# Kernel tuning notes

Measured on AMD Instinct MI355X. Metric: run time of the kernel, lower is better.

Reference implementation:

```python
import jax, jax.numpy as jnp
import numpy as np

ALPHA = 0.2  # LeakyReLU negative slope
NEG_INF = -9e15


def setup_inputs() -> dict:
    key = jax.random.key(0)
    k_h, k_adj, k_W, k_a = jax.random.split(key, 4)
    B, N, Din, Dout = 8, 1024, 256, 256
    h = jax.random.normal(k_h, (B, N, Din), dtype=jnp.float32)
    adj = jax.random.randint(k_adj, (B, N, N), 0, 2, dtype=jnp.int32)
    # nn.Linear weight [out, in], xavier-uniform-ish init for a
    W = jax.random.normal(k_W, (Dout, Din), dtype=jnp.float32) * (1.0 / np.sqrt(Din))
    lim = np.float32(1.414 * np.sqrt(6.0 / (2 * Dout + 1)))
    a = jax.random.uniform(k_a, (2 * Dout, 1), dtype=jnp.float32, minval=-lim, maxval=lim)
    return {"h": h, "adj": adj, "W": W, "a": a}


def reference(h, adj, W, a):
    # Wh: [B, N, F]
    Wh = jnp.einsum('bnd,fd->bnf', h, W)
    F_ = Wh.shape[-1]
    # Decompose concat-then-matmul: e_ij = leakyrelu(Wh_i @ a1 + Wh_j @ a2)
    a1 = a[:F_, 0]   # [F]
    a2 = a[F_:, 0]   # [F]
    src = Wh @ a1    # [B, N]  score contribution of row node i
    dst = Wh @ a2    # [B, N]  score contribution of col node j
    e = src[:, :, None] + dst[:, None, :]          # [B, N, N]
    e = jnp.where(e > 0, e, ALPHA * e)             # LeakyReLU
    e = jnp.where(adj > 0, e, NEG_INF)             # mask non-edges
    attention = jax.nn.softmax(e, axis=-1)         # [B, N, N]
    # dropout p=0.0 -> identity in eval/train
    h_prime = jnp.einsum('bij,bjf->bif', attention, Wh)
    return h_prime
```

## Files before the change

kernel.cpp:

```cpp
#include <hip/hip_runtime.h>
#include <hip/hip_bf16.h>
#include <cstdint>

#define ALPHA 0.2f
#define NEG_INF -9000000000000000.0f

typedef __bf16 bf16_t;
typedef __bf16 bf16x8 __attribute__((ext_vector_type(8)));
typedef float f32x16 __attribute__((ext_vector_type(16)));

__global__ __launch_bounds__(256) void k_gemm1(
    const float* __restrict__ h, const float* __restrict__ W, bf16_t* __restrict__ WhT)
{
  __shared__ bf16_t WS[64 * 72];
  __shared__ bf16_t HS[64 * 72];
  const int bx = blockIdx.x;
  const int b  = bx & 7;
  const int jt = (bx >> 3) & 15;
  const int ft = bx >> 7;
  const int j0 = jt * 64, f0 = ft * 64;
  const int t = threadIdx.x;
  const int w = t >> 6, lane = t & 63;
  const int mrow = lane & 31, half = lane >> 5;
  const int fsub = (w & 1) * 32, jsub = (w >> 1) * 32;

  const int lr = t >> 2;
  const int lc = (t & 3) * 16;
  const float* wp = W + ((size_t)(f0 + lr)) * 256 + lc;
  const float* hp = h + ((size_t)(b * 1024 + j0 + lr)) * 256 + lc;

  f32x16 acc;
#pragma unroll
  for (int r = 0; r < 16; r++) acc[r] = 0.f;

  for (int s = 0; s < 4; s++) {
    if (s) __syncthreads();
    {
      float4 w0 = *(const float4*)(wp + s * 64);
      float4 w1 = *(const float4*)(wp + s * 64 + 4);
      float4 w2 = *(const float4*)(wp + s * 64 + 8);
      float4 w3 = *(const float4*)(wp + s * 64 + 12);
      bf16x8 va, vb;
      va[0] = (bf16_t)w0.x; va[1] = (bf16_t)w0.y; va[2] = (bf16_t)w0.z; va[3] = (bf16_t)w0.w;
      va[4] = (bf16_t)w1.x; va[5] = (bf16_t)w1.y; va[6] = (bf16_t)w1.z; va[7] = (bf16_t)w1.w;
      vb[0] = (bf16_t)w2.x; vb[1] = (bf16_t)w2.y; vb[2] = (bf16_t)w2.z; vb[3] = (bf16_t)w2.w;
      vb[4] = (bf16_t)w3.x; vb[5] = (bf16_t)w3.y; vb[6] = (bf16_t)w3.z; vb[7] = (bf16_t)w3.w;
      *(bf16x8*)&WS[lr * 72 + lc] = va;
      *(bf16x8*)&WS[lr * 72 + lc + 8] = vb;
      float4 h0 = *(const float4*)(hp + s * 64);
      float4 h1 = *(const float4*)(hp + s * 64 + 4);
      float4 h2 = *(const float4*)(hp + s * 64 + 8);
      float4 h3 = *(const float4*)(hp + s * 64 + 12);
      bf16x8 vc, vd;
      vc[0] = (bf16_t)h0.x; vc[1] = (bf16_t)h0.y; vc[2] = (bf16_t)h0.z; vc[3] = (bf16_t)h0.w;
      vc[4] = (bf16_t)h1.x; vc[5] = (bf16_t)h1.y; vc[6] = (bf16_t)h1.z; vc[7] = (bf16_t)h1.w;
      vd[0] = (bf16_t)h2.x; vd[1] = (bf16_t)h2.y; vd[2] = (bf16_t)h2.z; vd[3] = (bf16_t)h2.w;
      vd[4] = (bf16_t)h3.x; vd[5] = (bf16_t)h3.y; vd[6] = (bf16_t)h3.z; vd[7] = (bf16_t)h3.w;
      *(bf16x8*)&HS[lr * 72 + lc] = vc;
      *(bf16x8*)&HS[lr * 72 + lc + 8] = vd;
    }
    __syncthreads();
#pragma unroll
    for (int ks = 0; ks < 4; ks++) {
      bf16x8 af = *(const bf16x8*)&WS[(fsub + mrow) * 72 + ks * 16 + half * 8];
      bf16x8 bf = *(const bf16x8*)&HS[(jsub + mrow) * 72 + ks * 16 + half * 8];
      acc = __builtin_amdgcn_mfma_f32_32x32x16_bf16(af, bf, acc, 0, 0, 0);
    }
  }

  const int jcol = j0 + jsub + mrow;
#pragma unroll
  for (int r = 0; r < 16; r++) {
    int frow = fsub + (r & 3) + 8 * (r >> 2) + 4 * half;
    WhT[(((size_t)(b * 256 + f0 + frow)) << 10) + jcol] = (bf16_t)acc[r];
  }
}

__global__ __launch_bounds__(256) void k_src(
    const float* __restrict__ h, const float* __restrict__ W, const float* __restrict__ a,
    float* __restrict__ src, float* __restrict__ dst)
{
  __shared__ float uS[512];
  const int t = threadIdx.x;
  {
    float s1a = 0.f, s1b = 0.f, s2a = 0.f, s2b = 0.f;
#pragma unroll 4
    for (int f = 0; f < 256; f += 2) {
      float w0 = W[f * 256 + t];
      float w1 = W[(f + 1) * 256 + t];
      s1a = fmaf(w0, a[f], s1a);       s1b = fmaf(w1, a[f + 1], s1b);
      s2a = fmaf(w0, a[256 + f], s2a); s2b = fmaf(w1, a[256 + f + 1], s2b);
    }
    uS[t] = s1a + s1b; uS[256 + t] = s2a + s2b;
  }
  __syncthreads();
  const int n = t >> 4, c = t & 15;
  const int m = blockIdx.x * 16 + n;
  const float* hp = h + (size_t)m * 256 + c * 16;
  float s1 = 0.f, s2 = 0.f;
#pragma unroll
  for (int i = 0; i < 4; i++) {
    float4 v = *(const float4*)(hp + i * 4);
    const float* u1p = &uS[c * 16 + i * 4];
    const float* u2p = &uS[256 + c * 16 + i * 4];
    s1 = fmaf(v.x, u1p[0], s1); s1 = fmaf(v.y, u1p[1], s1);
    s1 = fmaf(v.z, u1p[2], s1); s1 = fmaf(v.w, u1p[3], s1);
    s2 = fmaf(v.x, u2p[0], s2); s2 = fmaf(v.y, u2p[1], s2);
    s2 = fmaf(v.z, u2p[2], s2); s2 = fmaf(v.w, u2p[3], s2);
  }
#pragma unroll
  for (int off = 8; off; off >>= 1) {
    s1 += __shfl_down(s1, off, 16);
    s2 += __shfl_down(s2, off, 16);
  }
  if (c == 0) { src[m] = s1; dst[m] = s2; }
}

__global__ __launch_bounds__(256) void k_stats(
    const int* __restrict__ adj, const float* __restrict__ src, const float* __restrict__ dst,
    float* __restrict__ linv_ws, unsigned long long* __restrict__ mask_ws)
{
  const int b  = blockIdx.x & 7;
  const int i0 = (blockIdx.x >> 3) << 2;
  const int t  = threadIdx.x;
  const int wv = t >> 6, lane = t & 63;
  __shared__ float dstS[1024];
  __shared__ float srcS[4];
  __shared__ float partL[4][4];
  *(float4*)&dstS[t * 4] = *(const float4*)(dst + (b << 10) + t * 4);
  if (t < 4) srcS[t] = src[(b << 10) + i0 + t];
  __syncthreads();

  for (int i = 0; i < 4; i++) {
    float si = srcS[i];
    const size_t row = (size_t)(b << 10) + i0 + i;
    const int4 av = *(const int4*)(adj + (row << 10) + 4 * t);
    float4 dj = *(const float4*)&dstS[4 * t];
    float v0 = si + dj.x, v1 = si + dj.y, v2 = si + dj.z, v3 = si + dj.w;
    float e0 = (av.x > 0) ? fmaxf(v0, ALPHA * v0) : NEG_INF;
    float e1 = (av.y > 0) ? fmaxf(v1, ALPHA * v1) : NEG_INF;
    float e2 = (av.z > 0) ? fmaxf(v2, ALPHA * v2) : NEG_INF;
    float e3 = (av.w > 0) ? fmaxf(v3, ALPHA * v3) : NEG_INF;
    unsigned long long b0 = __ballot(av.x > 0);
    unsigned long long b1 = __ballot(av.y > 0);
    unsigned long long b2 = __ballot(av.z > 0);
    unsigned long long b3 = __ballot(av.w > 0);
    if (lane == 0) {
      unsigned long long* mp = mask_ws + row * 16 + wv * 4;
      mp[0] = b0; mp[1] = b1; mp[2] = b2; mp[3] = b3;
    }
    float lt = (__expf(e0) + __expf(e1)) + (__expf(e2) + __expf(e3));
#pragma unroll
    for (int off = 32; off; off >>= 1)
      lt += __shfl_down(lt, off, 64);
    if (lane == 0) partL[i][wv] = lt;
  }
  __syncthreads();
  if (t < 4) {
    float L = (partL[t][0] + partL[t][1]) + (partL[t][2] + partL[t][3]);
    linv_ws[(b << 10) + i0 + t] = 1.0f / L;
  }
}

__global__ __launch_bounds__(256) void k_attn(
    const bf16_t* __restrict__ WhT, const float* __restrict__ src, const float* __restrict__ dst,
    const float* __restrict__ linv_ws, const unsigned long long* __restrict__ mask_ws,
    float* __restrict__ out)
{
  const int b  = blockIdx.x & 7;
  const int fh = (blockIdx.x >> 3) & 1;
  const int i0 = (blockIdx.x >> 4) << 5;
  const int t  = threadIdx.x;
  const int w  = t >> 6;
  const int lane = t & 63;
  const int mrow = lane & 31, half = lane >> 5;

  __shared__ float dstS[1024];
  __shared__ float srcS[32], lInvS[32];
  __shared__ unsigned long long maskS[32 * 16];
  __shared__ bf16_t P[2][32 * 264];

  *(float4*)&dstS[t * 4] = *(const float4*)(dst + (b << 10) + t * 4);
  if (t < 32) {
    srcS[t]  = src[(b << 10) + i0 + t];
    lInvS[t] = linv_ws[(b << 10) + i0 + t];
  }
  {
    const size_t mb = ((size_t)(b << 10) + i0) * 16;
    maskS[t]       = mask_ws[mb + t];
    maskS[t + 256] = mask_ws[mb + t + 256];
  }
  __syncthreads();

  f32x16 acc;
#pragma unroll
  for (int r = 0; r < 16; r++) acc[r] = 0.f;

  const bf16_t* bp = WhT + (((size_t)(b * 256 + fh * 128 + w * 32 + mrow)) << 10);

  for (int c = 0; c < 4; c++) {
    bf16_t* Pc = &P[c & 1][0];
    {
      float dj = dstS[c * 256 + t];
      int mi = c * 4 + (t & 3);
      int sh = t >> 2;
#pragma unroll 8
      for (int i = 0; i < 32; i++) {
        unsigned long long w64 = maskS[i * 16 + mi];
        float v = srcS[i] + dj;
        float vl = fmaxf(v, ALPHA * v);
        float e = ((w64 >> sh) & 1ull) ? vl : NEG_INF;
        Pc[i * 264 + t] = (bf16_t)__expf(e);
      }
    }
    __syncthreads();

    const bf16_t* bpc = bp + c * 256 + half * 8;
    const bf16_t* prow = Pc + mrow * 264 + half * 8;
#pragma unroll
    for (int idx = 0; idx < 16; idx++) {
      bf16x8 bfr = *(const bf16x8*)(bpc + idx * 16);
      bf16x8 afr = *(const bf16x8*)(prow + idx * 16);
      acc = __builtin_amdgcn_mfma_f32_32x32x16_bf16(afr, bfr, acc, 0, 0, 0);
    }
  }

  const int col = fh * 128 + w * 32 + mrow;
#pragma unroll
  for (int r = 0; r < 16; r++) {
    int row = (r & 3) + 8 * (r >> 2) + 4 * half;
    out[((size_t)(b << 10) + i0 + row) * 256 + col] = acc[r] * lInvS[row];
  }
}

extern "C" void kernel_launch(void* const* d_in, const int* in_sizes, int n_in,
                              void* d_out, int out_size, void* d_ws, size_t ws_size,
                              hipStream_t stream) {
  const float* h   = (const float*)d_in[0];
  const int*   adj = (const int*)d_in[1];
  const float* W   = (const float*)d_in[2];
  const float* a   = (const float*)d_in[3];
  float* out = (float*)d_out;

  char* wsb = (char*)d_ws;
  bf16_t* WhT = (bf16_t*)wsb;
  float* srcv = (float*)(wsb + (4u << 20));
  float* dstv = srcv + 8192;
  float* linv = srcv + 16384;
  unsigned long long* mask_ws = (unsigned long long*)(wsb + (4u << 20) + 131072);

  k_gemm1<<<512,  256, 0, stream>>>(h, W, WhT);
  k_src  <<<512,  256, 0, stream>>>(h, W, a, srcv, dstv);
  k_stats<<<2048, 256, 0, stream>>>(adj, srcv, dstv, linv, mask_ws);
  k_attn <<<512,  256, 0, stream>>>(WhT, srcv, dstv, linv, mask_ws, out);
}
```

Baseline: 122.8 us.

## Materialize bf16 attention probabilities in stats kernel and stream them into attn GEMM

The stats kernel now writes exp'd masked scores as a bf16 P matrix to workspace instead of an edge bitmask. The attention kernel drops its LDS score recomputation and synchronization and feeds MFMA directly from global P and WhT. This removes redundant exp work and barriers but adds a large global write and read of the probability matrix. The src and gemm1 launches are also reordered.

Measured after the change: 137.5 us. 11.9% more time.

```diff
diff --git a/kernel.cpp b/kernel.cpp
--- a/kernel.cpp
+++ b/kernel.cpp
@@ -6,6 +6,7 @@
 #define NEG_INF -9000000000000000.0f
 
 typedef __bf16 bf16_t;
+typedef __bf16 bf16x4 __attribute__((ext_vector_type(4)));
 typedef __bf16 bf16x8 __attribute__((ext_vector_type(8)));
 typedef float f32x16 __attribute__((ext_vector_type(16)));
 
@@ -118,7 +119,7 @@
 
 __global__ __launch_bounds__(256) void k_stats(
     const int* __restrict__ adj, const float* __restrict__ src, const float* __restrict__ dst,
-    float* __restrict__ linv_ws, unsigned long long* __restrict__ mask_ws)
+    bf16_t* __restrict__ P, float* __restrict__ linv_ws)
 {
   const int b  = blockIdx.x & 7;
   const int i0 = (blockIdx.x >> 3) << 2;
@@ -131,25 +132,21 @@
   if (t < 4) srcS[t] = src[(b << 10) + i0 + t];
   __syncthreads();
 
+  const float4 dj = *(const float4*)&dstS[4 * t];
   for (int i = 0; i < 4; i++) {
-    float si = srcS[i];
+    const float si = srcS[i];
     const size_t row = (size_t)(b << 10) + i0 + i;
     const int4 av = *(const int4*)(adj + (row << 10) + 4 * t);
-    float4 dj = *(const float4*)&dstS[4 * t];
     float v0 = si + dj.x, v1 = si + dj.y, v2 = si + dj.z, v3 = si + dj.w;
     float e0 = (av.x > 0) ? fmaxf(v0, ALPHA * v0) : NEG_INF;
     float e1 = (av.y > 0) ? fmaxf(v1, ALPHA * v1) : NEG_INF;
     float e2 = (av.z > 0) ? fmaxf(v2, ALPHA * v2) : NEG_INF;
     float e3 = (av.w > 0) ? fmaxf(v3, ALPHA * v3) : NEG_INF;
-    unsigned long long b0 = __ballot(av.x > 0);
-    unsigned long long b1 = __ballot(av.y > 0);
-    unsigned long long b2 = __ballot(av.z > 0);
-    unsigned long long b3 = __ballot(av.w > 0);
-    if (lane == 0) {
-      unsigned long long* mp = mask_ws + row * 16 + wv * 4;
-      mp[0] = b0; mp[1] = b1; mp[2] = b2; mp[3] = b3;
-    }
-    float lt = (__expf(e0) + __expf(e1)) + (__expf(e2) + __expf(e3));
+    float x0 = __expf(e0), x1 = __expf(e1), x2 = __expf(e2), x3 = __expf(e3);
+    bf16x4 pv;
+    pv[0] = (bf16_t)x0; pv[1] = (bf16_t)x1; pv[2] = (bf16_t)x2; pv[3] = (bf16_t)x3;
+    *(bf16x4*)(P + (row << 10) + 4 * t) = pv;
+    float lt = (x0 + x1) + (x2 + x3);
 #pragma unroll
     for (int off = 32; off; off >>= 1)
       lt += __shfl_down(lt, off, 64);
@@ -163,9 +160,8 @@
 }
 
 __global__ __launch_bounds__(256) void k_attn(
-    const bf16_t* __restrict__ WhT, const float* __restrict__ src, const float* __restrict__ dst,
-    const float* __restrict__ linv_ws, const unsigned long long* __restrict__ mask_ws,
-    float* __restrict__ out)
+    const bf16_t* __restrict__ P, const bf16_t* __restrict__ WhT,
+    const float* __restrict__ linv_ws, float* __restrict__ out)
 {
   const int b  = blockIdx.x & 7;
   const int fh = (blockIdx.x >> 3) & 1;
@@ -175,61 +171,26 @@
   const int lane = t & 63;
   const int mrow = lane & 31, half = lane >> 5;
 
-  __shared__ float dstS[1024];
-  __shared__ float srcS[32], lInvS[32];
-  __shared__ unsigned long long maskS[32 * 16];
-  __shared__ bf16_t P[2][32 * 264];
-
-  *(float4*)&dstS[t * 4] = *(const float4*)(dst + (b << 10) + t * 4);
-  if (t < 32) {
-    srcS[t]  = src[(b << 10) + i0 + t];
-    lInvS[t] = linv_ws[(b << 10) + i0 + t];
-  }
-  {
-    const size_t mb = ((size_t)(b << 10) + i0) * 16;
-    maskS[t]       = mask_ws[mb + t];
-    maskS[t + 256] = mask_ws[mb + t + 256];
-  }
-  __syncthreads();
+  const bf16_t* ap = P + (((size_t)((b << 10) + i0 + mrow)) << 10) + half * 8;
+  const bf16_t* bp = WhT + (((size_t)(b * 256 + fh * 128 + w * 32 + mrow)) << 10) + half * 8;
 
   f32x16 acc;
 #pragma unroll
   for (int r = 0; r < 16; r++) acc[r] = 0.f;
 
-  const bf16_t* bp = WhT + (((size_t)(b * 256 + fh * 128 + w * 32 + mrow)) << 10);
-
-  for (int c = 0; c < 4; c++) {
-    bf16_t* Pc = &P[c & 1][0];
-    {
-      float dj = dstS[c * 256 + t];
-      int mi = c * 4 + (t & 3);
-      int sh = t >> 2;
 #pragma unroll 8
-      for (int i = 0; i < 32; i++) {
-        unsigned long long w64 = maskS[i * 16 + mi];
-        float v = srcS[i] + dj;
-        float vl = fmaxf(v, ALPHA * v);
-        float e = ((w64 >> sh) & 1ull) ? vl : NEG_INF;
-        Pc[i * 264 + t] = (bf16_t)__expf(e);
-      }
-    }
-    __syncthreads();
-
-    const bf16_t* bpc = bp + c * 256 + half * 8;
-    const bf16_t* prow = Pc + mrow * 264 + half * 8;
-#pragma unroll
-    for (int idx = 0; idx < 16; idx++) {
-      bf16x8 bfr = *(const bf16x8*)(bpc + idx * 16);
-      bf16x8 afr = *(const bf16x8*)(prow + idx * 16);
-      acc = __builtin_amdgcn_mfma_f32_32x32x16_bf16(afr, bfr, acc, 0, 0, 0);
-    }
+  for (int idx = 0; idx < 64; idx++) {
+    bf16x8 afr = *(const bf16x8*)(ap + idx * 16);
+    bf16x8 bfr = *(const bf16x8*)(bp + idx * 16);
+    acc = __builtin_amdgcn_mfma_f32_32x32x16_bf16(afr, bfr, acc, 0, 0, 0);
   }
 
   const int col = fh * 128 + w * 32 + mrow;
+  const float* lp = linv_ws + (b << 10) + i0;
 #pragma unroll
   for (int r = 0; r < 16; r++) {
     int row = (r & 3) + 8 * (r >> 2) + 4 * half;
-    out[((size_t)(b << 10) + i0 + row) * 256 + col] = acc[r] * lInvS[row];
+    out[((size_t)(b << 10) + i0 + row) * 256 + col] = acc[r] * lp[row];
   }
 }
 
@@ -244,13 +205,13 @@
 
   char* wsb = (char*)d_ws;
   bf16_t* WhT = (bf16_t*)wsb;
-  float* srcv = (float*)(wsb + (4u << 20));
+  bf16_t* P   = (bf16_t*)(wsb + (4u << 20));
+  float* srcv = (float*)(wsb + (20u << 20));
   float* dstv = srcv + 8192;
   float* linv = srcv + 16384;
-  unsigned long long* mask_ws = (unsigned long long*)(wsb + (4u << 20) + 131072);
-
+
+  k_src  <<<512,  256, 0, stream>>>(h, W, a, srcv, dstv);
   k_gemm1<<<512,  256, 0, stream>>>(h, W, WhT);
-  k_src  <<<512,  256, 0, stream>>>(h, W, a, srcv, dstv);
-  k_stats<<<2048, 256, 0, stream>>>(adj, srcv, dstv, linv, mask_ws);
-  k_attn <<<512,  256, 0, stream>>>(WhT, srcv, dstv, linv, mask_ws, out);
-}
+  k_stats<<<2048, 256, 0, stream>>>(adj, srcv, dstv, P, linv);
+  k_attn <<<512,  256, 0, stream>>>(P, WhT, linv, out);
+}
```
